# Optimization experiments

Measured on AMD Instinct MI355X. Metric: run time of the kernel, lower is better.

The kernel has to match this reference:

```python
import jax, jax.numpy as jnp
import numpy as np

# Model constants (from init_kwargs)
B, S, D = 2, 2048, 2048          # batch, seq, d_model
E = 64                           # num_routed_experts
TOP_K = 4
BOT = int(D * 0.25)              # bottle_dim = 512
EXP = 1536                       # routed expert hidden (bigmac_expert_size)
DFF = 8192                       # shared expert hidden (d_ff)
Z_LOSS_W = 1e-4
MOE_SCALE = 0.5                  # 1/(1 + [num_shared_experts>0])


def setup_inputs() -> dict:
    key = jax.random.key(0)
    ks = jax.random.split(key, 10)
    std = 0.011
    return {
        "x": jax.random.normal(ks[0], (B, S, D), jnp.float32),
        "router_w": jax.random.normal(ks[1], (E, D), jnp.float32) * 0.02,
        "gate_w": jax.random.normal(ks[2], (DFF, D), jnp.float32) * std,
        "up_w": jax.random.normal(ks[3], (DFF, D), jnp.float32) * std,
        "down_w": jax.random.normal(ks[4], (D, DFF), jnp.float32) * std,
        "w_down": jax.random.normal(ks[5], (BOT, D), jnp.float32) * std,
        "w_up": jax.random.normal(ks[6], (D, BOT), jnp.float32) * std,
        "w12": jax.random.normal(ks[7], (E, BOT, 2 * EXP), jnp.float32) * std,
        "w3": jax.random.normal(ks[8], (E, EXP, BOT), jnp.float32) * std,
    }


def reference(x, router_w, gate_w, up_w, down_w, w_down, w_up, w12, w3):
    b, s, d = x.shape
    h = x.reshape(-1, d)                       # [N, D]
    N = h.shape[0]
    NT = N * TOP_K                             # total routed token-slots

    # ---- router (fp32) ----
    logits = h @ router_w.T                    # [N, E]
    scores = jax.nn.sigmoid(logits)
    z_loss = jnp.mean(jnp.nan_to_num(logits) ** 2) * Z_LOSS_W
    # expert_bias is None -> selection_scores == scores
    _, topk_idx = jax.lax.top_k(scores, TOP_K)             # [N, K]
    topk_logits = jnp.take_along_axis(logits, topk_idx, axis=1)
    gating = jax.nn.softmax(topk_logits, axis=-1)          # [N, K]

    # ---- shared expert (SwiGLU) ----
    shared = (jax.nn.silu(h @ gate_w.T) * (h @ up_w.T)) @ down_w.T  # [N, D]

    # ---- bottleneck down-projection ----
    down = h @ w_down.T                        # [N, BOT]

    # ---- dispatch: sort tokens by expert, capacity-limited padding ----
    flat = topk_idx.reshape(-1)                # [NT]
    order = jnp.argsort(flat)                  # stable sort
    sorted_e = flat[order]
    counts = jax.ops.segment_sum(jnp.ones(NT, jnp.int32), flat, num_segments=E)
    ptr = jnp.cumsum(counts) - counts          # expert start offsets
    local = jnp.arange(NT) - ptr[sorted_e]     # rank within expert
    max_load = (NT // E // 8 + 6) * 8          # capacity per expert
    num_slots = E * max_load
    mask = local < max_load
    slots = sorted_e * max_load + local
    token_idx = jnp.repeat(jnp.arange(N), TOP_K)

    # reverse_map[slot] = source token row (N = dummy row); extra slot absorbs dropped tokens
    rev = jnp.full(num_slots + 1, N, dtype=jnp.int32)
    rev = rev.at[jnp.where(mask, slots, num_slots)].set(token_idx[order].astype(jnp.int32))
    rev = rev[:num_slots]

    h_dummy = jnp.concatenate([down, jnp.zeros((1, BOT), down.dtype)], axis=0)
    padding = h_dummy[rev].reshape(E, max_load, BOT)

    # ---- grouped expert GEMMs ----
    h12 = jnp.einsum('eld,edf->elf', padding, w12)   # [E, max_load, 2*EXP]
    h1, h2 = jnp.split(h12, 2, axis=-1)
    po = jnp.einsum('elf,efd->eld', jax.nn.silu(h1) * h2, w3)  # [E, max_load, BOT]
    po = jnp.concatenate([po.reshape(-1, BOT), jnp.zeros((1, BOT), po.dtype)], axis=0)

    # ---- combine: gather back, weight by gating ----
    gm = jnp.full(NT, num_slots, dtype=jnp.int32)
    gm = gm.at[order].set(jnp.where(mask, slots, num_slots).astype(jnp.int32))
    gathered = po[gm].reshape(N, TOP_K, BOT)
    routed = jnp.einsum('nk,nkd->nd', gating, gathered) @ w_up.T  # [N, D]

    # eval mode: route_scale = 1.0, aux_loss = 0
    out = ((shared + routed) * MOE_SCALE).reshape(b, s, d)
    return out, z_loss
```

## Files before the change

kernel.cpp:

```cpp
#include <hip/hip_runtime.h>

#define DEV __device__ __forceinline__

typedef __attribute__((ext_vector_type(4))) float f4;
typedef __attribute__((ext_vector_type(8))) __bf16 bfrag;
typedef __attribute__((ext_vector_type(4))) unsigned short us4;
typedef __attribute__((ext_vector_type(8))) unsigned short us8;

#define NTOK   4096
#define DMODEL 2048
#define NEXP   64
#define MAXLD  304
#define NSLOT  19456

DEV unsigned short f2bf(float f){
  union { float f; unsigned int i; } u; u.f = f;
  unsigned int r = u.i + 0x7fffu + ((u.i >> 16) & 1u);
  return (unsigned short)(r >> 16);
}
DEV float bf2f(unsigned short b){
  union { unsigned int i; float f; } u; u.i = ((unsigned int)b) << 16;
  return u.f;
}
DEV float silu_f(float g){ return g / (1.0f + __expf(-g)); }

DEV void gl_lds16(const unsigned short* g, unsigned short* l){
  __builtin_amdgcn_global_load_lds(
      (const __attribute__((address_space(1))) void*)g,
      (__attribute__((address_space(3))) void*)l, 16, 0, 0);
}

template<int BM, int EPI>
__global__ __launch_bounds__(512, 1) void gemm2(
    const unsigned short* __restrict__ A, const unsigned short* __restrict__ B,
    void* __restrict__ Cp, const float* __restrict__ add0, const float* __restrict__ add1,
    int M, int N, int K, int lda, int ldb,
    long long sA, long long sB, long long sC,
    void* __restrict__ Cp2, void* __restrict__ Cp3)
{
  constexpr int ALD = BM / 128;
  constexpr int MQ  = BM / 64;
  constexpr int HR  = BM / 2;
  __shared__ unsigned short As[2][2][HR * 64];
  __shared__ unsigned short Bs[2][2][128 * 64];

  A += (long long)blockIdx.z * sA;
  B += (long long)blockIdx.z * sB;
  const long long cbase = (long long)blockIdx.z * sC;

  const int nwg = gridDim.x * gridDim.y;
  int bid = blockIdx.y * gridDim.x + blockIdx.x;
  if ((nwg & 7) == 0) bid = (bid & 7) * (nwg >> 3) + (bid >> 3);
  const int bx = bid % gridDim.x, by = bid / gridDim.x;
  const int bm = by * BM, bn = bx * 256;

  const int t = threadIdx.x, lane = t & 63, wave = t >> 6;
  const int ha = wave >> 2;
  const int wn = (wave & 3) * 64;
  const int hb = wn >> 7;
  const int cb = wn & 127;
  const int fr = lane & 15, kg = lane >> 4;

  const int r0 = t >> 3;
  const int s0 = (t & 7) ^ (r0 & 7);

#define STG_AH(d_, h_, s_) do {                                                          \
    int rA0 = bm + (h_) * HR + r0; if (rA0 > M - 1) rA0 = M - 1;                         \
    gl_lds16(A + (long long)rA0 * lda + (long long)(s_) * 64 + s0 * 8,                   \
             &As[d_][h_][(wave * 64) * 8]);                                              \
    if (ALD == 2){                                                                       \
      int rA1 = bm + (h_) * HR + r0 + 64; if (rA1 > M - 1) rA1 = M - 1;                  \
      gl_lds16(A + (long long)rA1 * lda + (long long)(s_) * 64 + s0 * 8,                 \
               &As[d_][h_][(512 + wave * 64) * 8]);                                      \
    }                                                                                    \
  } while (0)
#define STG_BH(d_, h_, s_) do {                                                          \
    gl_lds16(B + (long long)(bn + (h_) * 128 + r0) * ldb + (long long)(s_) * 64 + s0 * 8,\
             &Bs[d_][h_][(wave * 64) * 8]);                                              \
    gl_lds16(B + (long long)(bn + (h_) * 128 + r0 + 64) * ldb + (long long)(s_) * 64 + s0 * 8, \
             &Bs[d_][h_][(512 + wave * 64) * 8]);                                        \
  } while (0)

  f4 acc[2 * MQ][4];
#pragma unroll
  for (int m = 0; m < 2 * MQ; ++m)
#pragma unroll
    for (int n = 0; n < 4; ++n) acc[m][n] = f4{0.f, 0.f, 0.f, 0.f};

  const int ns = K >> 6;

  STG_BH(0, 0, 0); STG_AH(0, 0, 0); STG_BH(0, 1, 0); STG_AH(0, 1, 0);
  STG_BH(1, 0, 1); STG_AH(1, 0, 1);
  asm volatile("s_waitcnt vmcnt(%0)" :: "i"(2 + ALD) : "memory");
  __builtin_amdgcn_s_barrier();

  for (int tt = 0; tt < ns; ++tt){
    const int d = tt & 1, nd = d ^ 1;
    bfrag af[MQ][2], bf[2][2][2];

#pragma unroll
    for (int ni = 0; ni < 2; ++ni)
#pragma unroll
      for (int kh = 0; kh < 2; ++kh){
        const int cn = cb + ni * 16 + fr;
        bf[0][ni][kh] = *(const bfrag*)&Bs[d][hb][cn * 64 + ((((kh << 2) | kg) ^ (cn & 7)) << 3)];
      }
#pragma unroll
    for (int mi = 0; mi < MQ; ++mi)
#pragma unroll
      for (int kh = 0; kh < 2; ++kh){
        const int rh = mi * 16 + fr;
        af[mi][kh] = *(const bfrag*)&As[d][ha][rh * 64 + ((((kh << 2) | kg) ^ (rh & 7)) << 3)];
      }
    if (tt + 1 < ns) STG_BH(nd, 1, tt + 1);
    if constexpr (BM == 256) asm volatile("s_waitcnt lgkmcnt(8)");
    else                     asm volatile("s_waitcnt lgkmcnt(4)");
    __builtin_amdgcn_s_barrier();
    asm volatile("s_waitcnt lgkmcnt(0)");
    __builtin_amdgcn_s_setprio(1);
#pragma unroll
    for (int mi = 0; mi < MQ; ++mi)
#pragma unroll
      for (int ni = 0; ni < 2; ++ni)
#pragma unroll
        for (int kh = 0; kh < 2; ++kh)
          acc[mi][ni] = __builtin_amdgcn_mfma_f32_16x16x32_bf16(af[mi][kh], bf[0][ni][kh], acc[mi][ni], 0, 0, 0);
    __builtin_amdgcn_s_setprio(0);
    __builtin_amdgcn_s_barrier();

#pragma unroll
    for (int ni = 0; ni < 2; ++ni)
#pragma unroll
      for (int kh = 0; kh < 2; ++kh){
        const int cn = cb + 32 + ni * 16 + fr;
        bf[1][ni][kh] = *(const bfrag*)&Bs[d][hb][cn * 64 + ((((kh << 2) | kg) ^ (cn & 7)) << 3)];
      }
    if (tt + 1 < ns) STG_AH(nd, 1, tt + 1);
    __builtin_amdgcn_s_barrier();
    asm volatile("s_waitcnt lgkmcnt(0)");
    __builtin_amdgcn_s_setprio(1);
#pragma unroll
    for (int mi = 0; mi < MQ; ++mi)
#pragma unroll
      for (int ni = 0; ni < 2; ++ni)
#pragma unroll
        for (int kh = 0; kh < 2; ++kh)
          acc[mi][2 + ni] = __builtin_amdgcn_mfma_f32_16x16x32_bf16(af[mi][kh], bf[1][ni][kh], acc[mi][2 + ni], 0, 0, 0);
    __builtin_amdgcn_s_setprio(0);
    __builtin_amdgcn_s_barrier();

#pragma unroll
    for (int mi = 0; mi < MQ; ++mi)
#pragma unroll
      for (int kh = 0; kh < 2; ++kh){
        const int rh = MQ * 16 + mi * 16 + fr;
        af[mi][kh] = *(const bfrag*)&As[d][ha][rh * 64 + ((((kh << 2) | kg) ^ (rh & 7)) << 3)];
      }
    if (tt + 2 < ns) STG_BH(d, 0, tt + 2);
    __builtin_amdgcn_s_barrier();
    asm volatile("s_waitcnt lgkmcnt(0)");
    __builtin_amdgcn_s_setprio(1);
#pragma unroll
    for (int mi = 0; mi < MQ; ++mi)
#pragma unroll
      for (int ni = 0; ni < 2; ++ni)
#pragma unroll
        for (int kh = 0; kh < 2; ++kh)
          acc[MQ + mi][2 + ni] = __builtin_amdgcn_mfma_f32_16x16x32_bf16(af[mi][kh], bf[1][ni][kh], acc[MQ + mi][2 + ni], 0, 0, 0);
    __builtin_amdgcn_s_setprio(0);
    __builtin_amdgcn_s_barrier();

    if (tt + 2 < ns) STG_AH(d, 0, tt + 2);
    __builtin_amdgcn_s_barrier();
    __builtin_amdgcn_s_setprio(1);
#pragma unroll
    for (int mi = 0; mi < MQ; ++mi)
#pragma unroll
      for (int ni = 0; ni < 2; ++ni)
#pragma unroll
        for (int kh = 0; kh < 2; ++kh)
          acc[MQ + mi][ni] = __builtin_amdgcn_mfma_f32_16x16x32_bf16(af[mi][kh], bf[0][ni][kh], acc[MQ + mi][ni], 0, 0, 0);
    __builtin_amdgcn_s_setprio(0);
    if (tt + 2 < ns)      asm volatile("s_waitcnt vmcnt(%0)" :: "i"(2 + ALD) : "memory");
    else if (tt + 1 < ns) asm volatile("s_waitcnt vmcnt(0)" ::: "memory");
    if (tt + 1 < ns) __builtin_amdgcn_s_barrier();
  }

  if constexpr (EPI == 3){
    const int base = bn + wn;
    if (base < 16384){
      const int colb = base >> 1;
#pragma unroll
      for (int mh = 0; mh < 2; ++mh)
#pragma unroll
        for (int mi = 0; mi < MQ; ++mi){
          const int row0 = bm + ha * HR + mh * (HR / 2) + mi * 16 + kg * 4;
#pragma unroll
          for (int p = 0; p < 2; ++p){
            f4 g = acc[mh * MQ + mi][2 * p];
            f4 u = acc[mh * MQ + mi][2 * p + 1];
#pragma unroll
            for (int r = 0; r < 4; ++r)
              ((unsigned short*)Cp)[(long long)(row0 + r) * 8192 + colb + p * 16 + fr]
                = f2bf(silu_f(g[r]) * u[r]);
          }
        }
    } else if (base < 16896){
      const int cb2 = base - 16384;
#pragma unroll
      for (int mh = 0; mh < 2; ++mh)
#pragma unroll
        for (int mi = 0; mi < MQ; ++mi){
          const int row0 = bm + ha * HR + mh * (HR / 2) + mi * 16 + kg * 4;
#pragma unroll
          for (int nf = 0; nf < 4; ++nf){
            f4 v = acc[mh * MQ + mi][nf];
#pragma unroll
            for (int r = 0; r < 4; ++r)
              ((unsigned short*)Cp2)[(long long)(row0 + r) * 512 + cb2 + nf * 16 + fr] = f2bf(v[r]);
          }
        }
    } else {
      const int cb3 = base - 16896;
#pragma unroll
      for (int mh = 0; mh < 2; ++mh)
#pragma unroll
        for (int mi = 0; mi < MQ; ++mi){
          const int row0 = bm + ha * HR + mh * (HR / 2) + mi * 16 + kg * 4;
#pragma unroll
          for (int nf = 0; nf < 4; ++nf){
            const int col = cb3 + nf * 16 + fr;
            f4 v = acc[mh * MQ + mi][nf];
            if (col < 64){
#pragma unroll
              for (int r = 0; r < 4; ++r)
                ((float*)Cp3)[(long long)(row0 + r) * 64 + col] = v[r];
            }
          }
        }
    }
    return;
  }
  if constexpr (EPI == 4){
    const int colb = (bn + wn) >> 1;
    const int ldo = N >> 1;
#pragma unroll
    for (int mh = 0; mh < 2; ++mh)
#pragma unroll
      for (int mi = 0; mi < MQ; ++mi){
        const int row0 = bm + ha * HR + mh * (HR / 2) + mi * 16 + kg * 4;
#pragma unroll
        for (int p = 0; p < 2; ++p){
          f4 g = acc[mh * MQ + mi][2 * p];
          f4 u = acc[mh * MQ + mi][2 * p + 1];
#pragma unroll
          for (int r = 0; r < 4; ++r){
            const int row = row0 + r;
            if (row < M)
              ((unsigned short*)Cp)[cbase + (long long)row * ldo + colb + p * 16 + fr]
                = f2bf(silu_f(g[r]) * u[r]);
          }
        }
      }
    return;
  }
#pragma unroll
  for (int mh = 0; mh < 2; ++mh)
#pragma unroll
    for (int mi = 0; mi < MQ; ++mi){
      const int row0 = bm + ha * HR + mh * (HR / 2) + mi * 16 + kg * 4;
#pragma unroll
      for (int nf = 0; nf < 4; ++nf){
        const int col = bn + wn + nf * 16 + fr;
        f4 v = acc[mh * MQ + mi][nf];
#pragma unroll
        for (int r = 0; r < 4; ++r){
          const int row = row0 + r;
          if (row < M){
            const long long off = cbase + (long long)row * N + col;
            if (EPI == 0)      ((unsigned short*)Cp)[off] = f2bf(v[r]);
            else if (EPI == 1) ((float*)Cp)[off] = v[r];
            else               ((float*)Cp)[off] = (v[r] + add0[off] + add1[off]) * 0.5f;
          }
        }
      }
    }
#undef STG_AH
#undef STG_BH
}

__global__ void cvt_bf16(const float* __restrict__ in, unsigned short* __restrict__ out,
                         long long n4)
{
  long long i = (long long)blockIdx.x * 256 + threadIdx.x;
  if (i >= n4) return;
  float4 v = ((const float4*)in)[i];
  us4 o; o[0] = f2bf(v.x); o[1] = f2bf(v.y); o[2] = f2bf(v.z); o[3] = f2bf(v.w);
  ((us4*)out)[i] = o;
}

__global__ void cvt_rowmap(const float* __restrict__ in, unsigned short* __restrict__ out,
                           int hi)
{
  const long long idx = (long long)blockIdx.x * 256 + threadIdx.x;
  const int row = (int)(idx >> 9);
  const int c4 = ((int)idx & 511) << 2;
  const int orow = ((row >> 4) << 5) | (hi << 4) | (row & 15);
  float4 v = *(const float4*)(in + (long long)row * 2048 + c4);
  us4 o; o[0] = f2bf(v.x); o[1] = f2bf(v.y); o[2] = f2bf(v.z); o[3] = f2bf(v.w);
  *(us4*)(out + (long long)orow * 2048 + c4) = o;
}

template<int MODE>
__global__ __launch_bounds__(256) void transpose_cvt(const float* __restrict__ in,
    unsigned short* __restrict__ out, int R, int C)
{
  __shared__ float tile[32][33];
  const long long z = blockIdx.z;
  const float* ip = in + z * (long long)R * C;
  unsigned short* op = out + z * (long long)R * C;
  const int r0 = blockIdx.y * 32, c0 = blockIdx.x * 32;
  const int t = threadIdx.x;
  const int lr = t >> 3, lc = (t & 7) * 4;
  float4 v = *(const float4*)(ip + (long long)(r0 + lr) * C + c0 + lc);
  tile[lr][lc+0] = v.x; tile[lr][lc+1] = v.y; tile[lr][lc+2] = v.z; tile[lr][lc+3] = v.w;
  __syncthreads();
  const int oc = t >> 3, orr = (t & 7) * 4;
  us4 o;
  o[0] = f2bf(tile[orr+0][oc]); o[1] = f2bf(tile[orr+1][oc]);
  o[2] = f2bf(tile[orr+2][oc]); o[3] = f2bf(tile[orr+3][oc]);
  int c = c0 + oc;
  int orow;
  if (MODE == 1)
    orow = (c < 1536) ? (((c >> 4) << 5) | (c & 15))
                      : ((((c - 1536) >> 4) << 5) | 16 | ((c - 1536) & 15));
  else
    orow = c;
  *(us4*)(op + (long long)orow * R + r0 + orr) = o;
}

__global__ void router_topk(const float* __restrict__ logits, int* __restrict__ topk,
                            float* __restrict__ gating, float* __restrict__ zout)
{
  const int t = threadIdx.x, w = t >> 6, lane = t & 63;
  const int n = blockIdx.x * 4 + w;
  const float lg = logits[(long long)n * 64 + lane];
  float z = lg * lg;
#pragma unroll
  for (int off = 32; off; off >>= 1) z += __shfl_xor(z, off);
  __shared__ float zs[4];
  if (lane == 0) zs[w] = z;
  __syncthreads();
  if (t == 0) atomicAdd(zout, (zs[0]+zs[1]+zs[2]+zs[3]) * (0.0001f / 262144.0f));

  float cur = lg;
  float tl[4]; int ti[4];
#pragma unroll
  for (int k = 0; k < 4; ++k){
    float s = cur; int si = lane;
#pragma unroll
    for (int off = 32; off; off >>= 1){
      float so = __shfl_xor(s, off); int io = __shfl_xor(si, off);
      if (so > s || (so == s && io < si)){ s = so; si = io; }
    }
    tl[k] = s; ti[k] = si;
    if (lane == si) cur = -3.0e38f;
  }
  if (lane == 0){
    const float m0 = tl[0];
    const float e0 = __expf(tl[0]-m0), e1 = __expf(tl[1]-m0),
                e2 = __expf(tl[2]-m0), e3 = __expf(tl[3]-m0);
    const float inv = 1.0f / (e0 + e1 + e2 + e3);
    topk[n*4+0] = ti[0]; topk[n*4+1] = ti[1]; topk[n*4+2] = ti[2]; topk[n*4+3] = ti[3];
    gating[n*4+0] = e0*inv; gating[n*4+1] = e1*inv; gating[n*4+2] = e2*inv; gating[n*4+3] = e3*inv;
  }
}

__global__ void scan_route(const int* __restrict__ topk, int* __restrict__ gm,
                           int* __restrict__ rev, int* __restrict__ counts)
{
  const int e = blockIdx.x;
  const int t = threadIdx.x, w = t >> 6, lane = t & 63;
  __shared__ int wtot[4];
  int running = 0;
  for (int c = 0; c < 16384; c += 256){
    const int j = c + t;
    const bool p = (topk[j] == e);
    const unsigned long long m = __ballot(p);
    const int prefix = __popcll(m & ((1ull << lane) - 1ull));
    if (lane == 0) wtot[w] = __popcll(m);
    __syncthreads();
    int woff = 0;
#pragma unroll
    for (int i = 0; i < 4; ++i){ if (i < w) woff += wtot[i]; }
    const int btot = wtot[0] + wtot[1] + wtot[2] + wtot[3];
    if (p){
      const int rank = running + woff + prefix;
      gm[j] = (rank < MAXLD) ? (e * MAXLD + rank) : NSLOT;
      if (rank < MAXLD) rev[e * MAXLD + rank] = j >> 2;
    }
    running += btot;
    __syncthreads();
  }
  if (t == 0) counts[e] = running;
}

__global__ void gather_pad(const unsigned short* __restrict__ down, const int* __restrict__ rev,
                           const int* __restrict__ counts, unsigned short* __restrict__ pad)
{
  const int idx = blockIdx.x * 256 + threadIdx.x;
  const int s = idx >> 6, c8 = (idx & 63) * 8;
  const int e = s / MAXLD;
  const int r = s - e * MAXLD;
  int cnt = counts[e]; if (cnt > MAXLD) cnt = MAXLD;
  us8 v = {0,0,0,0,0,0,0,0};
  if (r < cnt){
    const int tok = rev[s];
    v = *(const us8*)(down + (long long)tok * 512 + c8);
  }
  *(us8*)(pad + (long long)s * 512 + c8) = v;
}

__global__ void combine_moe(const unsigned short* __restrict__ po, const int* __restrict__ gm,
                            const float* __restrict__ gating, unsigned short* __restrict__ routed)
{
  const int idx = blockIdx.x * 256 + threadIdx.x;
  const int n = idx >> 6, c8 = (idx & 63) * 8;
  float acc[8] = {0,0,0,0,0,0,0,0};
#pragma unroll
  for (int k = 0; k < 4; ++k){
    const int slot = gm[n*4 + k];
    if (slot < NSLOT){
      const float gw = gating[n*4 + k];
      us8 v = *(const us8*)(po + (long long)slot * 512 + c8);
#pragma unroll
      for (int j = 0; j < 8; ++j) acc[j] += gw * bf2f(v[j]);
    }
  }
  us8 o;
#pragma unroll
  for (int j = 0; j < 8; ++j) o[j] = f2bf(acc[j]);
  *(us8*)(routed + (long long)n * 512 + c8) = o;
}

extern "C" void kernel_launch(void* const* d_in, const int* in_sizes, int n_in,
                              void* d_out, int out_size, void* d_ws, size_t ws_size,
                              hipStream_t stream)
{
  const float* x      = (const float*)d_in[0];
  const float* rw     = (const float*)d_in[1];
  const float* gate_w = (const float*)d_in[2];
  const float* up_w   = (const float*)d_in[3];
  const float* down_w = (const float*)d_in[4];
  const float* w_down = (const float*)d_in[5];
  const float* w_up   = (const float*)d_in[6];
  const float* w12    = (const float*)d_in[7];
  const float* w3     = (const float*)d_in[8];
  float* out = (float*)d_out;

  char* ws = (char*)d_ws;
  unsigned short* HBF   = (unsigned short*)(ws + 0ull);
  unsigned short* BBIG  = (unsigned short*)(ws + 16777216ull);
  unsigned short* DWB   = (unsigned short*)(ws + 87031808ull);
  unsigned short* WUB   = (unsigned short*)(ws + 120586240ull);
  unsigned short* W12I  = (unsigned short*)(ws + 122683392ull);
  unsigned short* W3T   = (unsigned short*)(ws + 324009984ull);
  float*          LOGIT = (float*)(ws + 424673280ull);
  int*            TOPKI = (int*)(ws + 425721856ull);
  float*          GATE4 = (float*)(ws + 425787392ull);
  int*            GM    = (int*)(ws + 425852928ull);
  int*            CNT   = (int*)(ws + 425918464ull);
  int*            REV   = (int*)(ws + 425919488ull);
  unsigned short* ACTS  = (unsigned short*)(ws + 426000384ull);
  unsigned short* AEXP  = (unsigned short*)(ws + 493109248ull);
  float*          SHRD  = (float*)(ws + 552878080ull);
  unsigned short* DNB   = (unsigned short*)(ws + 619987072ull);
  unsigned short* PAD   = (unsigned short*)(ws + 624181376ull);
  unsigned short* PO    = (unsigned short*)(ws + 644104192ull);
  unsigned short* RTD   = (unsigned short*)(ws + 664027136ull);

  hipMemsetAsync((char*)d_out + 8388608ull * 4, 0, 4, stream);
  hipMemsetAsync(BBIG + 16960ull * 2048, 0, 192ull * 2048 * 2, stream);

  cvt_bf16<<<8192,  256, 0, stream>>>(x, HBF, 2097152);
  cvt_rowmap<<<16384, 256, 0, stream>>>(gate_w, BBIG, 0);
  cvt_rowmap<<<16384, 256, 0, stream>>>(up_w,   BBIG, 1);
  cvt_bf16<<<1024,  256, 0, stream>>>(w_down, BBIG + 16384ull * 2048, 262144);
  cvt_bf16<<<128,   256, 0, stream>>>(rw,     BBIG + 16896ull * 2048, 32768);
  cvt_bf16<<<16384, 256, 0, stream>>>(down_w, DWB, 4194304);
  cvt_bf16<<<1024,  256, 0, stream>>>(w_up,   WUB, 262144);
  transpose_cvt<1><<<dim3(96,16,64), 256, 0, stream>>>(w12, W12I, 512, 3072);
  transpose_cvt<0><<<dim3(16,48,64), 256, 0, stream>>>(w3,  W3T,  1536, 512);

  gemm2<256,3><<<dim3(67,16,1), 512, 0, stream>>>(HBF, BBIG, ACTS, nullptr, nullptr,
      4096, 17152, 2048, 2048, 2048, 0, 0, 0, DNB, LOGIT);

  router_topk<<<1024, 256, 0, stream>>>(LOGIT, TOPKI, GATE4, out + 8388608);
  scan_route<<<64, 256, 0, stream>>>(TOPKI, GM, REV, CNT);

  gemm2<256,1><<<dim3(8,16,2), 512, 0, stream>>>(ACTS, DWB, SHRD, nullptr, nullptr,
      4096, 2048, 4096, 8192, 8192, 4096LL, 4096LL, 8388608LL, nullptr, nullptr);

  gather_pad<<<4864, 256, 0, stream>>>(DNB, REV, CNT, PAD);

  gemm2<128,4><<<dim3(12,3,64), 512, 0, stream>>>(PAD, W12I, AEXP, nullptr, nullptr,
      304, 3072, 512, 512, 512, 155648LL, 1572864LL, 466944LL, nullptr, nullptr);
  gemm2<128,0><<<dim3(2,3,64), 512, 0, stream>>>(AEXP, W3T, PO, nullptr, nullptr,
      304, 512, 1536, 1536, 1536, 466944LL, 786432LL, 155648LL, nullptr, nullptr);
  combine_moe<<<1024, 256, 0, stream>>>(PO, GM, GATE4, RTD);

  gemm2<128,2><<<dim3(8,32,1), 512, 0, stream>>>(RTD, WUB, out, SHRD, SHRD + 8388608,
      4096, 2048, 512, 512, 512, 0, 0, 0, nullptr, nullptr);
}
```

Before: 1.116 ms.

## Halve GEMM K-step, reshape LDS tiles, split-K shared down-proj into four bf16 partials

```diff
diff --git a/kernel.cpp b/kernel.cpp
--- a/kernel.cpp
+++ b/kernel.cpp
@@ -33,16 +33,15 @@
 template<int BM, int EPI>
 __global__ __launch_bounds__(512, 1) void gemm2(
     const unsigned short* __restrict__ A, const unsigned short* __restrict__ B,
-    void* __restrict__ Cp, const float* __restrict__ add0, const float* __restrict__ add1,
+    void* __restrict__ Cp, const unsigned short* __restrict__ part,
     int M, int N, int K, int lda, int ldb,
     long long sA, long long sB, long long sC,
     void* __restrict__ Cp2, void* __restrict__ Cp3)
 {
-  constexpr int ALD = BM / 128;
   constexpr int MQ  = BM / 64;
-  constexpr int HR  = BM / 2;
-  __shared__ unsigned short As[2][2][HR * 64];
-  __shared__ unsigned short Bs[2][2][128 * 64];
+  constexpr int NAH = (BM == 256) ? 2 : 1;
+  __shared__ unsigned short As[2][NAH][128 * 32];
+  __shared__ unsigned short Bs[2][2][128 * 32];
 
   A += (long long)blockIdx.z * sA;
   B += (long long)blockIdx.z * sB;
@@ -61,25 +60,17 @@
   const int cb = wn & 127;
   const int fr = lane & 15, kg = lane >> 4;
 
-  const int r0 = t >> 3;
-  const int s0 = (t & 7) ^ (r0 & 7);
-
-#define STG_AH(d_, h_, s_) do {                                                          \
-    int rA0 = bm + (h_) * HR + r0; if (rA0 > M - 1) rA0 = M - 1;                         \
-    gl_lds16(A + (long long)rA0 * lda + (long long)(s_) * 64 + s0 * 8,                   \
+  const int r0 = t >> 2;
+  const int s0 = (t & 3) ^ ((r0 >> 1) & 3);
+
+#define STG_A(d_, h_, s_) do {                                                           \
+    int rA = bm + (h_) * 128 + r0; if (rA > M - 1) rA = M - 1;                           \
+    gl_lds16(A + (long long)rA * lda + (long long)(s_) * 32 + s0 * 8,                    \
              &As[d_][h_][(wave * 64) * 8]);                                              \
-    if (ALD == 2){                                                                       \
-      int rA1 = bm + (h_) * HR + r0 + 64; if (rA1 > M - 1) rA1 = M - 1;                  \
-      gl_lds16(A + (long long)rA1 * lda + (long long)(s_) * 64 + s0 * 8,                 \
-               &As[d_][h_][(512 + wave * 64) * 8]);                                      \
-    }                                                                                    \
   } while (0)
-#define STG_BH(d_, h_, s_) do {                                                          \
-    gl_lds16(B + (long long)(bn + (h_) * 128 + r0) * ldb + (long long)(s_) * 64 + s0 * 8,\
-             &Bs[d_][h_][(wave * 64) * 8]);                                              \
-    gl_lds16(B + (long long)(bn + (h_) * 128 + r0 + 64) * ldb + (long long)(s_) * 64 + s0 * 8, \
-             &Bs[d_][h_][(512 + wave * 64) * 8]);                                        \
-  } while (0)
+#define STG_B(d_, h_, s_)                                                                \
+    gl_lds16(B + (long long)(bn + (h_) * 128 + r0) * ldb + (long long)(s_) * 32 + s0 * 8,\
+             &Bs[d_][h_][(wave * 64) * 8])
 
   f4 acc[2 * MQ][4];
 #pragma unroll
@@ -87,34 +78,36 @@
 #pragma unroll
     for (int n = 0; n < 4; ++n) acc[m][n] = f4{0.f, 0.f, 0.f, 0.f};
 
-  const int ns = K >> 6;
-
-  STG_BH(0, 0, 0); STG_AH(0, 0, 0); STG_BH(0, 1, 0); STG_AH(0, 1, 0);
-  STG_BH(1, 0, 1); STG_AH(1, 0, 1);
-  asm volatile("s_waitcnt vmcnt(%0)" :: "i"(2 + ALD) : "memory");
+  const int ns = K >> 5;
+
+  if constexpr (BM == 256){
+    STG_B(0, 0, 0); STG_A(0, 0, 0); STG_B(0, 1, 0); STG_A(0, 1, 0);
+    STG_B(1, 0, 1); STG_A(1, 0, 1);
+    asm volatile("s_waitcnt vmcnt(2)" ::: "memory");
+  } else {
+    STG_B(0, 0, 0); STG_A(0, 0, 0); STG_B(0, 1, 0);
+    STG_B(1, 0, 1);
+    asm volatile("s_waitcnt vmcnt(1)" ::: "memory");
+  }
   __builtin_amdgcn_s_barrier();
 
   for (int tt = 0; tt < ns; ++tt){
     const int d = tt & 1, nd = d ^ 1;
-    bfrag af[MQ][2], bf[2][2][2];
-
-#pragma unroll
-    for (int ni = 0; ni < 2; ++ni)
-#pragma unroll
-      for (int kh = 0; kh < 2; ++kh){
-        const int cn = cb + ni * 16 + fr;
-        bf[0][ni][kh] = *(const bfrag*)&Bs[d][hb][cn * 64 + ((((kh << 2) | kg) ^ (cn & 7)) << 3)];
-      }
-#pragma unroll
-    for (int mi = 0; mi < MQ; ++mi)
-#pragma unroll
-      for (int kh = 0; kh < 2; ++kh){
-        const int rh = mi * 16 + fr;
-        af[mi][kh] = *(const bfrag*)&As[d][ha][rh * 64 + ((((kh << 2) | kg) ^ (rh & 7)) << 3)];
-      }
-    if (tt + 1 < ns) STG_BH(nd, 1, tt + 1);
-    if constexpr (BM == 256) asm volatile("s_waitcnt lgkmcnt(8)");
-    else                     asm volatile("s_waitcnt lgkmcnt(4)");
+    bfrag af[MQ], bf[2][2];
+
+#pragma unroll
+    for (int ni = 0; ni < 2; ++ni){
+      const int cn = cb + ni * 16 + fr;
+      bf[0][ni] = *(const bfrag*)&Bs[d][hb][cn * 32 + ((kg ^ ((cn >> 1) & 3)) << 3)];
+    }
+#pragma unroll
+    for (int mi = 0; mi < MQ; ++mi){
+      const int rh = (BM == 256 ? mi * 16 : ha * 64 + mi * 16) + fr;
+      af[mi] = *(const bfrag*)&As[d][BM == 256 ? ha : 0][rh * 32 + ((kg ^ ((rh >> 1) & 3)) << 3)];
+    }
+    if (tt + 1 < ns) STG_B(nd, 1, tt + 1);
+    if constexpr (BM == 256) asm volatile("s_waitcnt lgkmcnt(4)");
+    else                     asm volatile("s_waitcnt lgkmcnt(2)");
     __builtin_amdgcn_s_barrier();
     asm volatile("s_waitcnt lgkmcnt(0)");
     __builtin_amdgcn_s_setprio(1);
@@ -122,20 +115,19 @@
     for (int mi = 0; mi < MQ; ++mi)
 #pragma unroll
       for (int ni = 0; ni < 2; ++ni)
-#pragma unroll
-        for (int kh = 0; kh < 2; ++kh)
-          acc[mi][ni] = __builtin_amdgcn_mfma_f32_16x16x32_bf16(af[mi][kh], bf[0][ni][kh], acc[mi][ni], 0, 0, 0);
+        acc[mi][ni] = __builtin_amdgcn_mfma_f32_16x16x32_bf16(af[mi], bf[0][ni], acc[mi][ni], 0, 0, 0);
     __builtin_amdgcn_s_setprio(0);
     __builtin_amdgcn_s_barrier();
 
 #pragma unroll
-    for (int ni = 0; ni < 2; ++ni)
-#pragma unroll
-      for (int kh = 0; kh < 2; ++kh){
-        const int cn = cb + 32 + ni * 16 + fr;
-        bf[1][ni][kh] = *(const bfrag*)&Bs[d][hb][cn * 64 + ((((kh << 2) | kg) ^ (cn & 7)) << 3)];
-      }
-    if (tt + 1 < ns) STG_AH(nd, 1, tt + 1);
+    for (int ni = 0; ni < 2; ++ni){
+      const int cn = cb + 32 + ni * 16 + fr;
+      bf[1][ni] = *(const bfrag*)&Bs[d][hb][cn * 32 + ((kg ^ ((cn >> 1) & 3)) << 3)];
+    }
+    if (tt + 1 < ns){
+      if constexpr (BM == 256) STG_A(nd, 1, tt + 1);
+      else                     STG_A(nd, 0, tt + 1);
+    }
     __builtin_amdgcn_s_barrier();
     asm volatile("s_waitcnt lgkmcnt(0)");
     __builtin_amdgcn_s_setprio(1);
@@ -143,20 +135,16 @@
     for (int mi = 0; mi < MQ; ++mi)
 #pragma unroll
       for (int ni = 0; ni < 2; ++ni)
-#pragma unroll
-        for (int kh = 0; kh < 2; ++kh)
-          acc[mi][2 + ni] = __builtin_amdgcn_mfma_f32_16x16x32_bf16(af[mi][kh], bf[1][ni][kh], acc[mi][2 + ni], 0, 0, 0);
+        acc[mi][2 + ni] = __builtin_amdgcn_mfma_f32_16x16x32_bf16(af[mi], bf[1][ni], acc[mi][2 + ni], 0, 0, 0);
     __builtin_amdgcn_s_setprio(0);
     __builtin_amdgcn_s_barrier();
 
 #pragma unroll
-    for (int mi = 0; mi < MQ; ++mi)
-#pragma unroll
-      for (int kh = 0; kh < 2; ++kh){
-        const int rh = MQ * 16 + mi * 16 + fr;
-        af[mi][kh] = *(const bfrag*)&As[d][ha][rh * 64 + ((((kh << 2) | kg) ^ (rh & 7)) << 3)];
-      }
-    if (tt + 2 < ns) STG_BH(d, 0, tt + 2);
+    for (int mi = 0; mi < MQ; ++mi){
+      const int rh = (BM == 256 ? 64 + mi * 16 : ha * 64 + 32 + mi * 16) + fr;
+      af[mi] = *(const bfrag*)&As[d][BM == 256 ? ha : 0][rh * 32 + ((kg ^ ((rh >> 1) & 3)) << 3)];
+    }
+    if (tt + 2 < ns) STG_B(d, 0, tt + 2);
     __builtin_amdgcn_s_barrier();
     asm volatile("s_waitcnt lgkmcnt(0)");
     __builtin_amdgcn_s_setprio(1);
@@ -164,25 +152,23 @@
     for (int mi = 0; mi < MQ; ++mi)
 #pragma unroll
       for (int ni = 0; ni < 2; ++ni)
-#pragma unroll
-        for (int kh = 0; kh < 2; ++kh)
-          acc[MQ + mi][2 + ni] = __builtin_amdgcn_mfma_f32_16x16x32_bf16(af[mi][kh], bf[1][ni][kh], acc[MQ + mi][2 + ni], 0, 0, 0);
+        acc[MQ + mi][2 + ni] = __builtin_amdgcn_mfma_f32_16x16x32_bf16(af[mi], bf[1][ni], acc[MQ + mi][2 + ni], 0, 0, 0);
     __builtin_amdgcn_s_setprio(0);
     __builtin_amdgcn_s_barrier();
 
-    if (tt + 2 < ns) STG_AH(d, 0, tt + 2);
+    if constexpr (BM == 256){ if (tt + 2 < ns) STG_A(d, 0, tt + 2); }
     __builtin_amdgcn_s_barrier();
     __builtin_amdgcn_s_setprio(1);
 #pragma unroll
     for (int mi = 0; mi < MQ; ++mi)
 #pragma unroll
       for (int ni = 0; ni < 2; ++ni)
-#pragma unroll
-        for (int kh = 0; kh < 2; ++kh)
-          acc[MQ + mi][ni] = __builtin_amdgcn_mfma_f32_16x16x32_bf16(af[mi][kh], bf[0][ni][kh], acc[MQ + mi][ni], 0, 0, 0);
+        acc[MQ + mi][ni] = __builtin_amdgcn_mfma_f32_16x16x32_bf16(af[mi], bf[0][ni], acc[MQ + mi][ni], 0, 0, 0);
     __builtin_amdgcn_s_setprio(0);
-    if (tt + 2 < ns)      asm volatile("s_waitcnt vmcnt(%0)" :: "i"(2 + ALD) : "memory");
-    else if (tt + 1 < ns) asm volatile("s_waitcnt vmcnt(0)" ::: "memory");
+    if (tt + 2 < ns){
+      if constexpr (BM == 256) asm volatile("s_waitcnt vmcnt(2)" ::: "memory");
+      else                     asm volatile("s_waitcnt vmcnt(1)" ::: "memory");
+    } else if (tt + 1 < ns)    asm volatile("s_waitcnt vmcnt(0)" ::: "memory");
     if (tt + 1 < ns) __builtin_amdgcn_s_barrier();
   }
 
@@ -194,7 +180,7 @@
       for (int mh = 0; mh < 2; ++mh)
 #pragma unroll
         for (int mi = 0; mi < MQ; ++mi){
-          const int row0 = bm + ha * HR + mh * (HR / 2) + mi * 16 + kg * 4;
+          const int row0 = bm + ha * (BM / 2) + mh * (BM / 4) + mi * 16 + kg * 4;
 #pragma unroll
           for (int p = 0; p < 2; ++p){
             f4 g = acc[mh * MQ + mi][2 * p];
@@ -211,7 +197,7 @@
       for (int mh = 0; mh < 2; ++mh)
 #pragma unroll
         for (int mi = 0; mi < MQ; ++mi){
-          const int row0 = bm + ha * HR + mh * (HR / 2) + mi * 16 + kg * 4;
+          const int row0 = bm + ha * (BM / 2) + mh * (BM / 4) + mi * 16 + kg * 4;
 #pragma unroll
           for (int nf = 0; nf < 4; ++nf){
             f4 v = acc[mh * MQ + mi][nf];
@@ -226,7 +212,7 @@
       for (int mh = 0; mh < 2; ++mh)
 #pragma unroll
         for (int mi = 0; mi < MQ; ++mi){
-          const int row0 = bm + ha * HR + mh * (HR / 2) + mi * 16 + kg * 4;
+          const int row0 = bm + ha * (BM / 2) + mh * (BM / 4) + mi * 16 + kg * 4;
 #pragma unroll
           for (int nf = 0; nf < 4; ++nf){
             const int col = cb3 + nf * 16 + fr;
@@ -248,7 +234,7 @@
     for (int mh = 0; mh < 2; ++mh)
 #pragma unroll
       for (int mi = 0; mi < MQ; ++mi){
-        const int row0 = bm + ha * HR + mh * (HR / 2) + mi * 16 + kg * 4;
+        const int row0 = bm + ha * (BM / 2) + mh * (BM / 4) + mi * 16 + kg * 4;
 #pragma unroll
         for (int p = 0; p < 2; ++p){
           f4 g = acc[mh * MQ + mi][2 * p];
@@ -268,7 +254,7 @@
   for (int mh = 0; mh < 2; ++mh)
 #pragma unroll
     for (int mi = 0; mi < MQ; ++mi){
-      const int row0 = bm + ha * HR + mh * (HR / 2) + mi * 16 + kg * 4;
+      const int row0 = bm + ha * (BM / 2) + mh * (BM / 4) + mi * 16 + kg * 4;
 #pragma unroll
       for (int nf = 0; nf < 4; ++nf){
         const int col = bn + wn + nf * 16 + fr;
@@ -280,13 +266,18 @@
             const long long off = cbase + (long long)row * N + col;
             if (EPI == 0)      ((unsigned short*)Cp)[off] = f2bf(v[r]);
             else if (EPI == 1) ((float*)Cp)[off] = v[r];
-            else               ((float*)Cp)[off] = (v[r] + add0[off] + add1[off]) * 0.5f;
+            else {
+              float s = v[r];
+#pragma unroll
+              for (int z = 0; z < 4; ++z) s += bf2f(part[(long long)z * 8388608 + off]);
+              ((float*)Cp)[off] = s * 0.5f;
+            }
           }
         }
       }
     }
-#undef STG_AH
-#undef STG_BH
+#undef STG_A
+#undef STG_B
 }
 
 __global__ void cvt_bf16(const float* __restrict__ in, unsigned short* __restrict__ out,
@@ -473,7 +464,7 @@
   int*            REV   = (int*)(ws + 425919488ull);
   unsigned short* ACTS  = (unsigned short*)(ws + 426000384ull);
   unsigned short* AEXP  = (unsigned short*)(ws + 493109248ull);
-  float*          SHRD  = (float*)(ws + 552878080ull);
+  unsigned short* SHRD  = (unsigned short*)(ws + 552878080ull);
   unsigned short* DNB   = (unsigned short*)(ws + 619987072ull);
   unsigned short* PAD   = (unsigned short*)(ws + 624181376ull);
   unsigned short* PO    = (unsigned short*)(ws + 644104192ull);
@@ -492,23 +483,23 @@
   transpose_cvt<1><<<dim3(96,16,64), 256, 0, stream>>>(w12, W12I, 512, 3072);
   transpose_cvt<0><<<dim3(16,48,64), 256, 0, stream>>>(w3,  W3T,  1536, 512);
 
-  gemm2<256,3><<<dim3(67,16,1), 512, 0, stream>>>(HBF, BBIG, ACTS, nullptr, nullptr,
+  gemm2<256,3><<<dim3(67,16,1), 512, 0, stream>>>(HBF, BBIG, ACTS, nullptr,
       4096, 17152, 2048, 2048, 2048, 0, 0, 0, DNB, LOGIT);
 
   router_topk<<<1024, 256, 0, stream>>>(LOGIT, TOPKI, GATE4, out + 8388608);
   scan_route<<<64, 256, 0, stream>>>(TOPKI, GM, REV, CNT);
 
-  gemm2<256,1><<<dim3(8,16,2), 512, 0, stream>>>(ACTS, DWB, SHRD, nullptr, nullptr,
-      4096, 2048, 4096, 8192, 8192, 4096LL, 4096LL, 8388608LL, nullptr, nullptr);
+  gemm2<256,0><<<dim3(8,16,4), 512, 0, stream>>>(ACTS, DWB, SHRD, nullptr,
+      4096, 2048, 2048, 8192, 8192, 2048LL, 2048LL, 8388608LL, nullptr, nullptr);
 
   gather_pad<<<4864, 256, 0, stream>>>(DNB, REV, CNT, PAD);
 
-  gemm2<128,4><<<dim3(12,3,64), 512, 0, stream>>>(PAD, W12I, AEXP, nullptr, nullptr,
+  gemm2<128,4><<<dim3(12,3,64), 512, 0, stream>>>(PAD, W12I, AEXP, nullptr,
       304, 3072, 512, 512, 512, 155648LL, 1572864LL, 466944LL, nullptr, nullptr);
-  gemm2<128,0><<<dim3(2,3,64), 512, 0, stream>>>(AEXP, W3T, PO, nullptr, nullptr,
+  gemm2<128,0><<<dim3(2,3,64), 512, 0, stream>>>(AEXP, W3T, PO, nullptr,
       304, 512, 1536, 1536, 1536, 466944LL, 786432LL, 155648LL, nullptr, nullptr);
   combine_moe<<<1024, 256, 0, stream>>>(PO, GM, GATE4, RTD);
 
-  gemm2<128,2><<<dim3(8,32,1), 512, 0, stream>>>(RTD, WUB, out, SHRD, SHRD + 8388608,
+  gemm2<128,2><<<dim3(8,32,1), 512, 0, stream>>>(RTD, WUB, out, SHRD,
       4096, 2048, 512, 512, 512, 0, 0, 0, nullptr, nullptr);
 }
```

Result: slower. 1.233 ms (+10.6%).
